# Performance work log

Hardware: AMD Instinct MI355X
Metric: run time of the kernel (lower is better)

The kernel has to match this reference:

```python
import jax, jax.numpy as jnp
import numpy as np

N_E = 1024
E_DIM = 64
BETA = 0.25


def setup_inputs() -> dict:
    key = jax.random.key(0)
    k1, k2 = jax.random.split(key)
    z = jax.random.normal(k1, (32, 32, 32, E_DIM), dtype=jnp.float32)
    # torch init: uniform(-1/n_e, 1/n_e)
    codebook = jax.random.uniform(k2, (N_E, E_DIM), dtype=jnp.float32,
                                  minval=-1.0 / N_E, maxval=1.0 / N_E)
    return {"z": z, "codebook": codebook}


def reference(z, codebook):
    z_flat = z.reshape(-1, E_DIM)  # [N, e_dim]
    # squared euclidean distances: ||z||^2 + ||e||^2 - 2 z e^T
    d = (jnp.sum(z_flat ** 2, axis=1, keepdims=True)
         + jnp.sum(codebook ** 2, axis=1)
         - 2.0 * jnp.matmul(z_flat, codebook.T))  # [N, n_e]
    idx = jnp.argmin(d, axis=1)  # [N]
    z_q = codebook[idx].reshape(z.shape)
    sg = jax.lax.stop_gradient
    loss = jnp.mean((sg(z_q) - z) ** 2) + BETA * jnp.mean((z_q - sg(z)) ** 2)
    z_q_st = z + sg(z_q - z)  # straight-through estimator
    return z_q_st, idx, loss
```

## Files before the change

kernel.cpp:

```cpp
#include <hip/hip_runtime.h>

#define NROWS 32768
#define NE    1024
#define ED    64
#define CHUNK 128
#define NCH   (NE / CHUNK)
#define RPW   8
#define NW    8
#define RPB   (RPW * NW)

typedef float4 f4;
typedef float2 f2;

__global__ void vq_prep(const float* __restrict__ cb, float* __restrict__ ssq)
{
    int j = blockIdx.x * blockDim.x + threadIdx.x;
    const f4* crow = (const f4*)(cb + (size_t)j * ED);
    float v[ED];
#pragma unroll
    for (int i = 0; i < 16; ++i) {
        f4 t = crow[i];
        v[4*i+0] = t.x; v[4*i+1] = t.y; v[4*i+2] = t.z; v[4*i+3] = t.w;
    }
    {
#pragma clang fp contract(off)
        float r0 = v[0]*v[0], r1 = v[1]*v[1], r2 = v[2]*v[2], r3 = v[3]*v[3];
        float r4 = v[4]*v[4], r5 = v[5]*v[5], r6 = v[6]*v[6], r7 = v[7]*v[7];
#pragma unroll
        for (int i = 8; i < ED; i += 8) {
            r0 += v[i+0]*v[i+0]; r1 += v[i+1]*v[i+1];
            r2 += v[i+2]*v[i+2]; r3 += v[i+3]*v[i+3];
            r4 += v[i+4]*v[i+4]; r5 += v[i+5]*v[i+5];
            r6 += v[i+6]*v[i+6]; r7 += v[i+7]*v[i+7];
        }
        ssq[j] = ((r0+r1)+(r2+r3)) + ((r4+r5)+(r6+r7));
    }
}

__global__ __launch_bounds__(512, 8)
void vq_main(const float* __restrict__ z, const float* __restrict__ cb,
             const float* __restrict__ ssq, float* __restrict__ out,
             float* __restrict__ partials)
{
    __shared__ __align__(16) float et[ED * CHUNK];
    __shared__ __align__(16) float sqsh[NE];
    __shared__ int   idxsh[RPB];
    __shared__ float wsum[NW];

    const int tid  = threadIdx.x;
    const int lane = tid & 63;
    const int w    = tid >> 6;
    const int w_u  = __builtin_amdgcn_readfirstlane(w);
    const int rowbase = blockIdx.x * RPB;

    if (tid < 256) ((f4*)sqsh)[tid] = ((const f4*)ssq)[tid];

    float cn[RPW];
    {
        const int rl = lane >> 3;
        const int jj = lane & 7;
        const float* zr = z + (size_t)(rowbase + w_u * RPW + rl) * ED;
        float a;
        {
#pragma clang fp contract(off)
            a = 0.f;
#pragma unroll
            for (int i = 0; i < 8; ++i) { float v = zr[8*i + jj]; a += v*v; }
        }
        a += __shfl_xor(a, 1);
        a += __shfl_xor(a, 2);
        a += __shfl_xor(a, 4);
#pragma unroll
        for (int r = 0; r < RPW; ++r) cn[r] = __shfl(a, r * 8);
    }

    float bestv[RPW];
    int   besti[RPW];
#pragma unroll
    for (int r = 0; r < RPW; ++r) { bestv[r] = INFINITY; besti[r] = 0; }

    const f2* et2 = (const f2*)et;
    const float* zw = z + (size_t)(rowbase + w_u * RPW) * ED;

    for (int ch = 0; ch < NCH; ++ch) {
        __syncthreads();
        {
            const int c = tid & 127;
            const int h = tid >> 7;
            const f4* crow = (const f4*)(cb + (size_t)(ch * CHUNK + c) * ED
                                         + h * 16);
#pragma unroll
            for (int i = 0; i < 4; ++i) {
                f4 t = crow[i];
                const int dim = h * 16 + 4 * i;
                et[(dim+0) * CHUNK + c] = t.x;
                et[(dim+1) * CHUNK + c] = t.y;
                et[(dim+2) * CHUNK + c] = t.z;
                et[(dim+3) * CHUNK + c] = t.w;
            }
        }
        __syncthreads();

        f2 sv = ((const f2*)sqsh)[ch * 64 + lane];
        float svq[2] = {sv.x, sv.y};

        float acc[RPW][2];
#pragma unroll
        for (int r = 0; r < RPW; ++r) acc[r][0] = acc[r][1] = 0.f;

#pragma unroll 2
        for (int k4 = 0; k4 < 16; ++k4) {
            f2 e0 = et2[(4*k4+0) * 64 + lane];
            f2 e1 = et2[(4*k4+1) * 64 + lane];
            f2 e2 = et2[(4*k4+2) * 64 + lane];
            f2 e3 = et2[(4*k4+3) * 64 + lane];
            f4 z0 = *(const f4*)(zw + 0*ED + 4*k4);
            f4 z1 = *(const f4*)(zw + 1*ED + 4*k4);
            f4 z2 = *(const f4*)(zw + 2*ED + 4*k4);
            f4 z3 = *(const f4*)(zw + 3*ED + 4*k4);
            f4 z4 = *(const f4*)(zw + 4*ED + 4*k4);
            f4 z5 = *(const f4*)(zw + 5*ED + 4*k4);
            f4 z6 = *(const f4*)(zw + 6*ED + 4*k4);
            f4 z7 = *(const f4*)(zw + 7*ED + 4*k4);
#define ROWFMA(r, zz)                                                    \
            acc[r][0] = fmaf(zz.x, e0.x, acc[r][0]);                     \
            acc[r][1] = fmaf(zz.x, e0.y, acc[r][1]);                     \
            acc[r][0] = fmaf(zz.y, e1.x, acc[r][0]);                     \
            acc[r][1] = fmaf(zz.y, e1.y, acc[r][1]);                     \
            acc[r][0] = fmaf(zz.z, e2.x, acc[r][0]);                     \
            acc[r][1] = fmaf(zz.z, e2.y, acc[r][1]);                     \
            acc[r][0] = fmaf(zz.w, e3.x, acc[r][0]);                     \
            acc[r][1] = fmaf(zz.w, e3.y, acc[r][1]);
            ROWFMA(0, z0) ROWFMA(1, z1) ROWFMA(2, z2) ROWFMA(3, z3)
            ROWFMA(4, z4) ROWFMA(5, z5) ROWFMA(6, z6) ROWFMA(7, z7)
#undef ROWFMA
        }

        {
#pragma clang fp contract(off)
#pragma unroll
            for (int r = 0; r < RPW; ++r) {
#pragma unroll
                for (int q = 0; q < 2; ++q) {
                    float t1 = cn[r] + svq[q];
                    float d  = t1 - 2.0f * acc[r][q];
                    int j = ch * CHUNK + lane * 2 + q;
                    if (d < bestv[r]) { bestv[r] = d; besti[r] = j; }
                }
            }
        }
    }

    float lp = 0.f;
#pragma unroll
    for (int r = 0; r < RPW; ++r) {
        float v = bestv[r];
        int   i = besti[r];
#pragma unroll
        for (int m = 1; m < 64; m <<= 1) {
            float ov = __shfl_xor(v, m);
            int   oi = __shfl_xor(i, m);
            if (ov < v || (ov == v && oi < i)) { v = ov; i = oi; }
        }
        i &= (NE - 1);
        const int grow = rowbase + w * RPW + r;
        float zq, zz, diff, st;
        {
#pragma clang fp contract(off)
            zq   = cb[(size_t)i * ED + lane];
            zz   = z [(size_t)grow * ED + lane];
            diff = zq - zz;
            st   = zz + diff;
            lp  += diff * diff;
        }
        out[(size_t)grow * ED + lane] = st;
        if (lane == 0) idxsh[w * RPW + r] = i;
    }

#pragma unroll
    for (int m = 1; m < 64; m <<= 1) lp += __shfl_xor(lp, m);
    if (lane == 0) wsum[w] = lp;
    __syncthreads();

    if (tid < RPB) {
        int iv = idxsh[tid] & (NE - 1);
        out[(size_t)NROWS * ED + rowbase + tid] = (float)iv;
    }
    if (tid == 0)
        partials[blockIdx.x] = (((wsum[0]+wsum[1]) + (wsum[2]+wsum[3]))
                              + ((wsum[4]+wsum[5]) + (wsum[6]+wsum[7])));
}

__global__ void vq_finalize(const float* __restrict__ partials,
                            float* __restrict__ out)
{
    __shared__ float red[256];
    int t = threadIdx.x;
    red[t] = partials[t] + partials[t + 256];
    __syncthreads();
    for (int m = 128; m > 0; m >>= 1) {
        if (t < m) red[t] += red[t + m];
        __syncthreads();
    }
    if (t == 0) {
        float mean = red[0] / (float)((size_t)NROWS * ED);
        out[(size_t)NROWS * ED + NROWS] = mean + 0.25f * mean;
    }
}

extern "C" void kernel_launch(void* const* d_in, const int* in_sizes, int n_in,
                              void* d_out, int out_size, void* d_ws, size_t ws_size,
                              hipStream_t stream)
{
    (void)in_sizes; (void)n_in; (void)out_size; (void)ws_size;
    const float* z  = (const float*)d_in[0];
    const float* cb = (const float*)d_in[1];
    float* out = (float*)d_out;
    float* ssq      = (float*)d_ws;
    float* partials = ssq + NE;

    vq_prep<<<4, 256, 0, stream>>>(cb, ssq);
    vq_main<<<512, 512, 0, stream>>>(z, cb, ssq, out, partials);
    vq_finalize<<<1, 256, 0, stream>>>(partials, out);
}
```

Measured before the change: 92.35 us.

## Halve rows per wave and double grid to 1024 blocks

Cuts rows per wave from 8 to 4 and doubles the grid to 1024 blocks, so more blocks spread over the CUs. The finalize kernel is changed to reduce 1024 partials. The per-block shared norm table is dropped in favour of direct global loads, the launch-bounds occupancy hint is removed, and the inner loop unroll is raised. The trade-off is that each block still stages the full codebook through LDS, so codebook staging traffic per row doubles and data reuse per LDS load halves.

Result: faster. 84.70 us (-8.3%).

```diff
diff --git a/kernel.cpp b/kernel.cpp
--- a/kernel.cpp
+++ b/kernel.cpp
@@ -5,7 +5,7 @@
 #define ED    64
 #define CHUNK 128
 #define NCH   (NE / CHUNK)
-#define RPW   8
+#define RPW   4
 #define NW    8
 #define RPB   (RPW * NW)
 
@@ -16,34 +16,32 @@
 {
     int j = blockIdx.x * blockDim.x + threadIdx.x;
     const f4* crow = (const f4*)(cb + (size_t)j * ED);
-    float v[ED];
-#pragma unroll
-    for (int i = 0; i < 16; ++i) {
-        f4 t = crow[i];
-        v[4*i+0] = t.x; v[4*i+1] = t.y; v[4*i+2] = t.z; v[4*i+3] = t.w;
-    }
+    f4 v[16];
+#pragma unroll
+    for (int i = 0; i < 16; ++i) v[i] = crow[i];
     {
 #pragma clang fp contract(off)
-        float r0 = v[0]*v[0], r1 = v[1]*v[1], r2 = v[2]*v[2], r3 = v[3]*v[3];
-        float r4 = v[4]*v[4], r5 = v[5]*v[5], r6 = v[6]*v[6], r7 = v[7]*v[7];
-#pragma unroll
-        for (int i = 8; i < ED; i += 8) {
-            r0 += v[i+0]*v[i+0]; r1 += v[i+1]*v[i+1];
-            r2 += v[i+2]*v[i+2]; r3 += v[i+3]*v[i+3];
-            r4 += v[i+4]*v[i+4]; r5 += v[i+5]*v[i+5];
-            r6 += v[i+6]*v[i+6]; r7 += v[i+7]*v[i+7];
+        float r0 = v[0].x*v[0].x, r1 = v[0].y*v[0].y;
+        float r2 = v[0].z*v[0].z, r3 = v[0].w*v[0].w;
+        float r4 = v[1].x*v[1].x, r5 = v[1].y*v[1].y;
+        float r6 = v[1].z*v[1].z, r7 = v[1].w*v[1].w;
+#pragma unroll
+        for (int q = 2; q < 16; q += 2) {
+            r0 += v[q].x*v[q].x;     r1 += v[q].y*v[q].y;
+            r2 += v[q].z*v[q].z;     r3 += v[q].w*v[q].w;
+            r4 += v[q+1].x*v[q+1].x; r5 += v[q+1].y*v[q+1].y;
+            r6 += v[q+1].z*v[q+1].z; r7 += v[q+1].w*v[q+1].w;
         }
         ssq[j] = ((r0+r1)+(r2+r3)) + ((r4+r5)+(r6+r7));
     }
 }
 
-__global__ __launch_bounds__(512, 8)
+__global__ __launch_bounds__(512)
 void vq_main(const float* __restrict__ z, const float* __restrict__ cb,
              const float* __restrict__ ssq, float* __restrict__ out,
              float* __restrict__ partials)
 {
     __shared__ __align__(16) float et[ED * CHUNK];
-    __shared__ __align__(16) float sqsh[NE];
     __shared__ int   idxsh[RPB];
     __shared__ float wsum[NW];
 
@@ -53,13 +51,13 @@
     const int w_u  = __builtin_amdgcn_readfirstlane(w);
     const int rowbase = blockIdx.x * RPB;
 
-    if (tid < 256) ((f4*)sqsh)[tid] = ((const f4*)ssq)[tid];
+    const float* zw = z + (size_t)(rowbase + w_u * RPW) * ED;
 
     float cn[RPW];
     {
-        const int rl = lane >> 3;
+        const int rl = (lane >> 3) & 3;
         const int jj = lane & 7;
-        const float* zr = z + (size_t)(rowbase + w_u * RPW + rl) * ED;
+        const float* zr = zw + (size_t)rl * ED;
         float a;
         {
 #pragma clang fp contract(off)
@@ -80,7 +78,6 @@
     for (int r = 0; r < RPW; ++r) { bestv[r] = INFINITY; besti[r] = 0; }
 
     const f2* et2 = (const f2*)et;
-    const float* zw = z + (size_t)(rowbase + w_u * RPW) * ED;
 
     for (int ch = 0; ch < NCH; ++ch) {
         __syncthreads();
@@ -101,14 +98,14 @@
         }
         __syncthreads();
 
-        f2 sv = ((const f2*)sqsh)[ch * 64 + lane];
+        f2 sv = ((const f2*)(ssq + ch * CHUNK))[lane];
         float svq[2] = {sv.x, sv.y};
 
         float acc[RPW][2];
 #pragma unroll
         for (int r = 0; r < RPW; ++r) acc[r][0] = acc[r][1] = 0.f;
 
-#pragma unroll 2
+#pragma unroll 4
         for (int k4 = 0; k4 < 16; ++k4) {
             f2 e0 = et2[(4*k4+0) * 64 + lane];
             f2 e1 = et2[(4*k4+1) * 64 + lane];
@@ -118,10 +115,6 @@
             f4 z1 = *(const f4*)(zw + 1*ED + 4*k4);
             f4 z2 = *(const f4*)(zw + 2*ED + 4*k4);
             f4 z3 = *(const f4*)(zw + 3*ED + 4*k4);
-            f4 z4 = *(const f4*)(zw + 4*ED + 4*k4);
-            f4 z5 = *(const f4*)(zw + 5*ED + 4*k4);
-            f4 z6 = *(const f4*)(zw + 6*ED + 4*k4);
-            f4 z7 = *(const f4*)(zw + 7*ED + 4*k4);
 #define ROWFMA(r, zz)                                                    \
             acc[r][0] = fmaf(zz.x, e0.x, acc[r][0]);                     \
             acc[r][1] = fmaf(zz.x, e0.y, acc[r][1]);                     \
@@ -132,7 +125,6 @@
             acc[r][0] = fmaf(zz.w, e3.x, acc[r][0]);                     \
             acc[r][1] = fmaf(zz.w, e3.y, acc[r][1]);
             ROWFMA(0, z0) ROWFMA(1, z1) ROWFMA(2, z2) ROWFMA(3, z3)
-            ROWFMA(4, z4) ROWFMA(5, z5) ROWFMA(6, z6) ROWFMA(7, z7)
 #undef ROWFMA
         }
 
@@ -196,7 +188,8 @@
 {
     __shared__ float red[256];
     int t = threadIdx.x;
-    red[t] = partials[t] + partials[t + 256];
+    float s = (partials[t] + partials[t + 256]) + (partials[t + 512] + partials[t + 768]);
+    red[t] = s;
     __syncthreads();
     for (int m = 128; m > 0; m >>= 1) {
         if (t < m) red[t] += red[t + m];
@@ -220,6 +213,6 @@
     float* partials = ssq + NE;
 
     vq_prep<<<4, 256, 0, stream>>>(cb, ssq);
-    vq_main<<<512, 512, 0, stream>>>(z, cb, ssq, out, partials);
+    vq_main<<<1024, 512, 0, stream>>>(z, cb, ssq, out, partials);
     vq_finalize<<<1, 256, 0, stream>>>(partials, out);
 }
```
